# Kernel optimization log

Measured on AMD Instinct MI355X. Metric: run time of the kernel, lower is better.

Reference implementation:

```python
import jax, jax.numpy as jnp
import numpy as np

B, N, C, H = 2, 2048, 1024, 16
D = C // H          # head dim = 64
HID = 4 * C         # MLP hidden = 4096
LN_EPS = 1e-5
ROPE_BASE = 10000.0


def layernorm(x, g, b):
    mu = jnp.mean(x, axis=-1, keepdims=True)
    var = jnp.var(x, axis=-1, keepdims=True)
    return (x - mu) * jax.lax.rsqrt(var + LN_EPS) * g + b


def rotate_half(x):
    # interleaved pairs: (x0, x1) -> (-x1, x0), lucidrains rotary_embedding_torch style
    x = x.reshape(*x.shape[:-1], -1, 2)
    x1, x2 = x[..., 0], x[..., 1]
    return jnp.stack([-x2, x1], axis=-1).reshape(*x.shape[:-2], -1)


def rope_cos_sin(n, d, dtype):
    inv_freq = 1.0 / (ROPE_BASE ** (jnp.arange(0, d, 2, dtype=jnp.float32) / d))
    ang = jnp.arange(n, dtype=jnp.float32)[:, None] * inv_freq          # [N, D/2]
    ang = jnp.repeat(ang, 2, axis=-1)                                    # [N, D] interleaved
    return jnp.cos(ang).astype(dtype), jnp.sin(ang).astype(dtype)


def setup_inputs() -> dict:
    key = jax.random.key(0)
    ks = jax.random.split(key, 16)
    s = 0.02
    return {
        "x": jax.random.normal(ks[0], (B, N, C), jnp.float32),
        "ln1_g": jnp.ones((C,), jnp.float32),
        "ln1_b": jnp.zeros((C,), jnp.float32),
        "qkv_w": jax.random.normal(ks[1], (C, 3 * C), jnp.float32) * s,   # stored [in, out]
        "qkv_b": jnp.zeros((3 * C,), jnp.float32),
        "proj_w": jax.random.normal(ks[2], (C, C), jnp.float32) * s,
        "proj_b": jnp.zeros((C,), jnp.float32),
        "ln2_g": jnp.ones((C,), jnp.float32),
        "ln2_b": jnp.zeros((C,), jnp.float32),
        "fc1_w": jax.random.normal(ks[3], (C, HID), jnp.float32) * s,
        "fc1_b": jnp.zeros((HID,), jnp.float32),
        "ffn_ln_g": jnp.ones((HID,), jnp.float32),
        "ffn_ln_b": jnp.zeros((HID,), jnp.float32),
        "fc2_w": jax.random.normal(ks[4], (HID, C), jnp.float32) * s,
        "fc2_b": jnp.zeros((C,), jnp.float32),
    }


def reference(x, ln1_g, ln1_b, qkv_w, qkv_b, proj_w, proj_b,
              ln2_g, ln2_b, fc1_w, fc1_b, ffn_ln_g, ffn_ln_b, fc2_w, fc2_b):
    b, n, c = x.shape
    h, d = H, c // H
    scale = d ** -0.5

    # --- attention branch (pre-norm) ---
    hx = layernorm(x, ln1_g, ln1_b)
    qkv = hx @ qkv_w + qkv_b                                   # [B,N,3C]
    qkv = qkv.reshape(b, n, 3, h, d).transpose(2, 0, 3, 1, 4)  # [3,B,H,N,D]
    q, k, v = qkv[0], qkv[1], qkv[2]

    cos, sin = rope_cos_sin(n, d, x.dtype)                     # [N,D]
    q = q * cos + rotate_half(q) * sin
    k = k * cos + rotate_half(k) * sin

    attn = jax.nn.softmax(jnp.einsum('bhqd,bhkd->bhqk', q, k) * scale, axis=-1)
    o = jnp.einsum('bhqk,bhkd->bhqd', attn, v)                 # [B,H,N,D]
    o = o.transpose(0, 2, 1, 3).reshape(b, n, c)               # B N (H D)
    x = x + o @ proj_w + proj_b

    # --- MLP branch (pre-norm; GELU then LayerNorm on hidden, per FeedForwardBlock) ---
    m = layernorm(x, ln2_g, ln2_b)
    m = jax.nn.gelu(m @ fc1_w + fc1_b, approximate=False)
    m = layernorm(m, ffn_ln_g, ffn_ln_b)
    m = m @ fc2_w + fc2_b
    return x + m
```

## Files before the change

kernel.cpp:

```cpp
#include <hip/hip_runtime.h>
#include <hip/hip_bf16.h>
#include <cmath>

typedef __bf16 bf16_t;
typedef __bf16 bf16x8 __attribute__((ext_vector_type(8)));
typedef float f32x4 __attribute__((ext_vector_type(4)));
typedef unsigned short u16;
typedef unsigned int u32;

__device__ __forceinline__ void load16(const bf16_t* g, bf16_t* l) {
  __builtin_amdgcn_global_load_lds((const __attribute__((address_space(1))) u32*)g,
                                   (__attribute__((address_space(3))) u32*)l, 16, 0, 0);
}

__device__ __forceinline__ u32 pk2(float a, float b) {
  bf16_t x = (bf16_t)a, y = (bf16_t)b;
  u16 ux = __builtin_bit_cast(u16, x), uy = __builtin_bit_cast(u16, y);
  return (u32)ux | ((u32)uy << 16);
}

union V4U { u32 w[4]; bf16x8 v; };

__global__ __launch_bounds__(256) void transpose_w(const float* __restrict__ Wsrc,
                                                   bf16_t* __restrict__ Wt, int Kd, int Nd) {
  __shared__ float tile[32][33];
  int n0 = blockIdx.x * 32, k0 = blockIdx.y * 32;
  int tx = threadIdx.x & 31, ty = threadIdx.x >> 5;
  for (int i = ty; i < 32; i += 8)
    tile[i][tx] = Wsrc[(size_t)(k0 + i) * Nd + n0 + tx];
  __syncthreads();
  for (int i = ty; i < 32; i += 8)
    Wt[(size_t)(n0 + i) * Kd + k0 + tx] = (bf16_t)tile[tx][i];
}

__global__ void rope_tab(float* __restrict__ c, float* __restrict__ s) {
  int pos = blockIdx.x, t = threadIdx.x;
  float e = (float)(2 * t) / 64.0f;
  float inv = powf(10000.0f, -e);
  float a = (float)pos * inv;
  c[pos * 32 + t] = cosf(a);
  s[pos * 32 + t] = sinf(a);
}

template <typename TI, int W>
__global__ __launch_bounds__(256) void ln_kernel(const TI* __restrict__ in,
                                                 const float* __restrict__ g,
                                                 const float* __restrict__ b,
                                                 bf16_t* __restrict__ out) {
  constexpr int PT = W / 256;
  int row = blockIdx.x;
  const TI* p = in + (size_t)row * W;
  float vals[PT];
  float s = 0.f, q = 0.f;
  for (int i = 0; i < PT; ++i) {
    float v = (float)p[threadIdx.x + i * 256];
    vals[i] = v; s += v; q += v * v;
  }
  for (int off = 32; off; off >>= 1) { s += __shfl_xor(s, off); q += __shfl_xor(q, off); }
  __shared__ float red[8];
  int wave = threadIdx.x >> 6, lane = threadIdx.x & 63;
  if (lane == 0) { red[wave] = s; red[4 + wave] = q; }
  __syncthreads();
  s = red[0] + red[1] + red[2] + red[3];
  q = red[4] + red[5] + red[6] + red[7];
  float mu = s * (1.0f / W);
  float var = q * (1.0f / W) - mu * mu;
  float rstd = rsqrtf(var + 1e-5f);
  bf16_t* op = out + (size_t)row * W;
  for (int i = 0; i < PT; ++i) {
    int cix = threadIdx.x + i * 256;
    op[cix] = (bf16_t)((vals[i] - mu) * rstd * g[cix] + b[cix]);
  }
}

enum { EPI_QKV = 0, EPI_RESID = 1, EPI_GELU = 2 };

template <int EPI>
__global__ __launch_bounds__(256, 2) void gemm_bt(
    const bf16_t* __restrict__ A, const bf16_t* __restrict__ Bt, int M, int Nn, int K,
    const float* __restrict__ bias, const float* __restrict__ resid,
    float* __restrict__ outf, bf16_t* __restrict__ outb,
    bf16_t* __restrict__ qb, bf16_t* __restrict__ kb, bf16_t* __restrict__ vtb,
    const float* __restrict__ ropeC, const float* __restrict__ ropeS) {
  __shared__ bf16_t lsA[128 * 32];
  __shared__ bf16_t lsB[128 * 32];
  const int tid = threadIdx.x;
  const int lane = tid & 63;
  const int wave = tid >> 6;
  const int l16 = lane & 15, quad = lane >> 4;
  const int wm = (wave >> 1) * 64, wn = (wave & 1) * 64;
  const int m0 = blockIdx.y * 128, n0 = blockIdx.x * 128;

  f32x4 acc[4][4];
  for (int i = 0; i < 4; ++i)
    for (int j = 0; j < 4; ++j) acc[i][j] = {0.f, 0.f, 0.f, 0.f};

  for (int kk = 0; kk < K; kk += 32) {
    __syncthreads();
    for (int i = 0; i < 2; ++i) {
      int s = tid + i * 256;
      int row = s >> 2, ch = s & 3;
      load16(A + (size_t)(m0 + row) * K + kk + ch * 8, lsA + s * 8);
      load16(Bt + (size_t)(n0 + row) * K + kk + ch * 8, lsB + s * 8);
    }
    __syncthreads();
    bf16x8 af[4], bfr[4];
    for (int t = 0; t < 4; ++t) {
      af[t] = *(const bf16x8*)(lsA + (wm + t * 16 + l16) * 32 + quad * 8);
      bfr[t] = *(const bf16x8*)(lsB + (wn + t * 16 + l16) * 32 + quad * 8);
    }
    for (int mt = 0; mt < 4; ++mt)
      for (int nt = 0; nt < 4; ++nt)
        acc[mt][nt] = __builtin_amdgcn_mfma_f32_16x16x32_bf16(af[mt], bfr[nt], acc[mt][nt], 0, 0, 0);
  }

  for (int mt = 0; mt < 4; ++mt) {
    for (int nt = 0; nt < 4; ++nt) {
      int gn = n0 + wn + nt * 16 + l16;
      int gm0 = m0 + wm + mt * 16 + quad * 4;
      if constexpr (EPI == EPI_QKV) {
        int which = gn >> 10;
        int hd = gn & 1023, head = hd >> 6, d = hd & 63;
        if (which == 2) {
          u32 lo, hi;
          {
            float v0 = acc[mt][nt][0] + bias[gn];
            float v1 = acc[mt][nt][1] + bias[gn];
            float v2 = acc[mt][nt][2] + bias[gn];
            float v3 = acc[mt][nt][3] + bias[gn];
            lo = pk2(v0, v1);
            hi = pk2(v2, v3);
          }
          int b = gm0 >> 11, pos = gm0 & 2047;
          int bh = b * 16 + head;
          uint2 pk; pk.x = lo; pk.y = hi;
          *(uint2*)(vtb + ((size_t)bh * 64 + d) * 2048 + pos) = pk;
        } else {
          bf16_t* dst = (which == 0) ? qb : kb;
          int t = d >> 1;
          for (int r = 0; r < 4; ++r) {
            float v = acc[mt][nt][r] + bias[gn];
            float pn = __shfl_xor(v, 1);
            int gm = gm0 + r;
            int b = gm >> 11, pos = gm & 2047;
            float cc = ropeC[pos * 32 + t], ss = ropeS[pos * 32 + t];
            float o = (d & 1) ? (v * cc + pn * ss) : (v * cc - pn * ss);
            dst[(((size_t)(b * 16 + head)) * 2048 + pos) * 64 + d] = (bf16_t)o;
          }
        }
      } else if constexpr (EPI == EPI_GELU) {
        for (int r = 0; r < 4; ++r) {
          int gm = gm0 + r;
          float v = acc[mt][nt][r] + bias[gn];
          float g = 0.5f * v * (1.0f + erff(v * 0.70710678118654752f));
          outb[(size_t)gm * Nn + gn] = (bf16_t)g;
        }
      } else {
        for (int r = 0; r < 4; ++r) {
          int gm = gm0 + r;
          size_t idx = (size_t)gm * Nn + gn;
          outf[idx] = acc[mt][nt][r] + bias[gn] + resid[idx];
        }
      }
    }
  }
}

__global__ __launch_bounds__(256, 2) void attn_kernel(
    const bf16_t* __restrict__ q, const bf16_t* __restrict__ k,
    const bf16_t* __restrict__ vt, bf16_t* __restrict__ o) {
  __shared__ bf16_t lsK[128 * 64];
  __shared__ bf16_t lsV[64 * 128];

  const int tid = threadIdx.x, lane = tid & 63, wave = tid >> 6;
  const int l16 = lane & 15, quad = lane >> 4;
  const int bh = blockIdx.y, qt = blockIdx.x;
  const int b = bh >> 4, h = bh & 15;
  const bf16_t* qp = q + (size_t)bh * 2048 * 64;
  const bf16_t* kp = k + (size_t)bh * 2048 * 64;
  const bf16_t* vp = vt + (size_t)bh * 64 * 2048;
  const int qrow0 = qt * 128 + wave * 32;

  bf16x8 qa[2][2];
#pragma unroll
  for (int mt = 0; mt < 2; ++mt)
#pragma unroll
    for (int ks = 0; ks < 2; ++ks) {
      bf16x8 t = *(const bf16x8*)(qp + (size_t)(qrow0 + mt * 16 + l16) * 64 + ks * 32 + quad * 8);
#pragma unroll
      for (int j = 0; j < 8; ++j) t[j] = (bf16_t)((float)t[j] * 0.125f);
      qa[mt][ks] = t;
    }

  f32x4 oacc[2][4];
#pragma unroll
  for (int i = 0; i < 2; ++i)
#pragma unroll
    for (int j = 0; j < 4; ++j) oacc[i][j] = {0.f, 0.f, 0.f, 0.f};
  float mstate[2] = {-1e30f, -1e30f};
  float lstate[2] = {0.f, 0.f};

  for (int kt = 0; kt < 16; ++kt) {
    __syncthreads();
    const bf16_t* kg = kp + (size_t)kt * 128 * 64;
#pragma unroll
    for (int i = 0; i < 4; ++i) {
      int s = tid + i * 256;
      int kr = s >> 3, kc = (s & 7) ^ (kr & 7);
      load16(kg + (size_t)kr * 64 + kc * 8, lsK + s * 8);
      int vr = s >> 4, vc = (s & 15) ^ (vr & 7);
      load16(vp + (size_t)vr * 2048 + kt * 128 + vc * 8, lsV + s * 8);
    }
    __syncthreads();

    f32x4 sacc[8][2];
#pragma unroll
    for (int nt = 0; nt < 8; ++nt)
#pragma unroll
      for (int mt = 0; mt < 2; ++mt) sacc[nt][mt] = {0.f, 0.f, 0.f, 0.f};
#pragma unroll
    for (int ks = 0; ks < 2; ++ks)
#pragma unroll
      for (int nt = 0; nt < 8; ++nt) {
        int rr = nt * 16 + l16;
        int cs = (ks * 4 + quad) ^ (rr & 7);
        bf16x8 kf = *(const bf16x8*)(lsK + rr * 64 + cs * 8);
        sacc[nt][0] = __builtin_amdgcn_mfma_f32_16x16x32_bf16(kf, qa[0][ks], sacc[nt][0], 0, 0, 0);
        sacc[nt][1] = __builtin_amdgcn_mfma_f32_16x16x32_bf16(kf, qa[1][ks], sacc[nt][1], 0, 0, 0);
      }

    u32 u[2][8][2];
#pragma unroll
    for (int mt = 0; mt < 2; ++mt) {
      float mx = sacc[0][mt][0];
#pragma unroll
      for (int nt = 0; nt < 8; ++nt)
#pragma unroll
        for (int r = 0; r < 4; ++r) mx = fmaxf(mx, sacc[nt][mt][r]);
      mx = fmaxf(mx, __shfl_xor(mx, 16));
      mx = fmaxf(mx, __shfl_xor(mx, 32));
      float mnew = fmaxf(mstate[mt], mx);
      float alpha = __expf(mstate[mt] - mnew);
      mstate[mt] = mnew;
      float rs = 0.f;
#pragma unroll
      for (int nt = 0; nt < 8; ++nt) {
        float p0 = __expf(sacc[nt][mt][0] - mnew);
        float p1 = __expf(sacc[nt][mt][1] - mnew);
        float p2 = __expf(sacc[nt][mt][2] - mnew);
        float p3 = __expf(sacc[nt][mt][3] - mnew);
        rs += (p0 + p1) + (p2 + p3);
        u[mt][nt][0] = pk2(p0, p1);
        u[mt][nt][1] = pk2(p2, p3);
      }
      rs += __shfl_xor(rs, 16);
      rs += __shfl_xor(rs, 32);
      lstate[mt] = lstate[mt] * alpha + rs;
#pragma unroll
      for (int r = 0; r < 4; ++r) {
        float a = __shfl(alpha, quad * 4 + r);
#pragma unroll
        for (int dt = 0; dt < 4; ++dt) oacc[mt][dt][r] *= a;
      }
    }

#pragma unroll
    for (int ks = 0; ks < 4; ++ks) {
      bf16x8 pf[2];
#pragma unroll
      for (int mt = 0; mt < 2; ++mt) {
        V4U a;
#pragma unroll
        for (int w = 0; w < 4; ++w) {
          int src = ((quad & 1) * 2 + (w >> 1)) * 16 + l16;
          u32 lo = (u32)__shfl((int)u[mt][2 * ks + 0][w & 1], src);
          u32 hi = (u32)__shfl((int)u[mt][2 * ks + 1][w & 1], src);
          a.w[w] = (quad & 2) ? hi : lo;
        }
        pf[mt] = a.v;
      }
#pragma unroll
      for (int dt = 0; dt < 4; ++dt) {
        int rd = dt * 16 + l16;
        int cs = (ks * 4 + quad) ^ (rd & 7);
        bf16x8 vf = *(const bf16x8*)(lsV + rd * 128 + cs * 8);
        oacc[0][dt] = __builtin_amdgcn_mfma_f32_16x16x32_bf16(pf[0], vf, oacc[0][dt], 0, 0, 0);
        oacc[1][dt] = __builtin_amdgcn_mfma_f32_16x16x32_bf16(pf[1], vf, oacc[1][dt], 0, 0, 0);
      }
    }
  }

#pragma unroll
  for (int mt = 0; mt < 2; ++mt) {
    float inv = 1.0f / lstate[mt];
#pragma unroll
    for (int r = 0; r < 4; ++r) {
      float li = __shfl(inv, quad * 4 + r);
      int row = qrow0 + mt * 16 + quad * 4 + r;
#pragma unroll
      for (int dt = 0; dt < 4; ++dt) {
        int d = dt * 16 + l16;
        o[((size_t)(b * 2048 + row)) * 1024 + h * 64 + d] = (bf16_t)(oacc[mt][dt][r] * li);
      }
    }
  }
}

extern "C" void kernel_launch(void* const* d_in, const int* in_sizes, int n_in,
                              void* d_out, int out_size, void* d_ws, size_t ws_size,
                              hipStream_t stream) {
  const float* x = (const float*)d_in[0];
  const float* ln1_g = (const float*)d_in[1];
  const float* ln1_b = (const float*)d_in[2];
  const float* qkv_w = (const float*)d_in[3];
  const float* qkv_b = (const float*)d_in[4];
  const float* proj_w = (const float*)d_in[5];
  const float* proj_b = (const float*)d_in[6];
  const float* ln2_g = (const float*)d_in[7];
  const float* ln2_b = (const float*)d_in[8];
  const float* fc1_w = (const float*)d_in[9];
  const float* fc1_b = (const float*)d_in[10];
  const float* ffg = (const float*)d_in[11];
  const float* ffb = (const float*)d_in[12];
  const float* fc2_w = (const float*)d_in[13];
  const float* fc2_b = (const float*)d_in[14];
  float* out = (float*)d_out;

  char* ws = (char*)d_ws;
  size_t off = 0;
  auto alloc = [&](size_t n) { char* p = ws + off; off += (n + 255) & ~(size_t)255; return p; };

  bf16_t* qkvT  = (bf16_t*)alloc(3072ull * 1024 * 2);
  bf16_t* projT = (bf16_t*)alloc(1024ull * 1024 * 2);
  bf16_t* fc1T  = (bf16_t*)alloc(4096ull * 1024 * 2);
  bf16_t* fc2T  = (bf16_t*)alloc(1024ull * 4096 * 2);
  float*  ropeC = (float*)alloc(2048ull * 32 * 4);
  float*  ropeS = (float*)alloc(2048ull * 32 * 4);
  bf16_t* hx    = (bf16_t*)alloc(4096ull * 1024 * 2);
  bf16_t* qbuf  = (bf16_t*)alloc(32ull * 2048 * 64 * 2);
  bf16_t* kbuf  = (bf16_t*)alloc(32ull * 2048 * 64 * 2);
  bf16_t* vtbuf = (bf16_t*)alloc(32ull * 64 * 2048 * 2);
  bf16_t* obuf  = (bf16_t*)alloc(4096ull * 1024 * 2);
  float*  x2    = (float*)alloc(4096ull * 1024 * 4);
  bf16_t* h1    = (bf16_t*)alloc(4096ull * 4096 * 2);
  bf16_t* hln   = (bf16_t*)qbuf;

  transpose_w<<<dim3(96, 32), 256, 0, stream>>>(qkv_w, qkvT, 1024, 3072);
  transpose_w<<<dim3(32, 32), 256, 0, stream>>>(proj_w, projT, 1024, 1024);
  transpose_w<<<dim3(128, 32), 256, 0, stream>>>(fc1_w, fc1T, 1024, 4096);
  transpose_w<<<dim3(32, 128), 256, 0, stream>>>(fc2_w, fc2T, 4096, 1024);
  rope_tab<<<2048, 32, 0, stream>>>(ropeC, ropeS);

  ln_kernel<float, 1024><<<4096, 256, 0, stream>>>(x, ln1_g, ln1_b, hx);
  gemm_bt<EPI_QKV><<<dim3(24, 32), 256, 0, stream>>>(hx, qkvT, 4096, 3072, 1024, qkv_b,
      nullptr, nullptr, nullptr, qbuf, kbuf, vtbuf, ropeC, ropeS);
  attn_kernel<<<dim3(16, 32), 256, 0, stream>>>(qbuf, kbuf, vtbuf, obuf);
  gemm_bt<EPI_RESID><<<dim3(8, 32), 256, 0, stream>>>(obuf, projT, 4096, 1024, 1024, proj_b,
      x, x2, nullptr, nullptr, nullptr, nullptr, nullptr, nullptr);
  ln_kernel<float, 1024><<<4096, 256, 0, stream>>>(x2, ln2_g, ln2_b, hx);
  gemm_bt<EPI_GELU><<<dim3(32, 32), 256, 0, stream>>>(hx, fc1T, 4096, 4096, 1024, fc1_b,
      nullptr, nullptr, h1, nullptr, nullptr, nullptr, nullptr, nullptr);
  ln_kernel<bf16_t, 4096><<<4096, 256, 0, stream>>>(h1, ffg, ffb, hln);
  gemm_bt<EPI_RESID><<<dim3(8, 32), 256, 0, stream>>>(hln, fc2T, 4096, 1024, 4096, fc2_b,
      x2, out, nullptr, nullptr, nullptr, nullptr, nullptr, nullptr);
}
```

Measured before the change: 432.2 us.

## Rewrite attention with 32x32 MFMA, double-buffered K/V, exp2 softmax

```diff
diff --git a/kernel.cpp b/kernel.cpp
--- a/kernel.cpp
+++ b/kernel.cpp
@@ -5,6 +5,7 @@
 typedef __bf16 bf16_t;
 typedef __bf16 bf16x8 __attribute__((ext_vector_type(8)));
 typedef float f32x4 __attribute__((ext_vector_type(4)));
+typedef float f32x16 __attribute__((ext_vector_type(16)));
 typedef unsigned short u16;
 typedef unsigned int u32;
 
@@ -169,141 +170,130 @@
 __global__ __launch_bounds__(256, 2) void attn_kernel(
     const bf16_t* __restrict__ q, const bf16_t* __restrict__ k,
     const bf16_t* __restrict__ vt, bf16_t* __restrict__ o) {
-  __shared__ bf16_t lsK[128 * 64];
-  __shared__ bf16_t lsV[64 * 128];
+  __shared__ bf16_t lsK[2][128 * 64];
+  __shared__ bf16_t lsV[2][64 * 128];
 
   const int tid = threadIdx.x, lane = tid & 63, wave = tid >> 6;
-  const int l16 = lane & 15, quad = lane >> 4;
+  const int c31 = lane & 31, hi = lane >> 5, h7 = c31 & 7;
   const int bh = blockIdx.y, qt = blockIdx.x;
   const int b = bh >> 4, h = bh & 15;
   const bf16_t* qp = q + (size_t)bh * 2048 * 64;
   const bf16_t* kp = k + (size_t)bh * 2048 * 64;
   const bf16_t* vp = vt + (size_t)bh * 64 * 2048;
   const int qrow0 = qt * 128 + wave * 32;
-
-  bf16x8 qa[2][2];
-#pragma unroll
-  for (int mt = 0; mt < 2; ++mt)
-#pragma unroll
-    for (int ks = 0; ks < 2; ++ks) {
-      bf16x8 t = *(const bf16x8*)(qp + (size_t)(qrow0 + mt * 16 + l16) * 64 + ks * 32 + quad * 8);
-#pragma unroll
-      for (int j = 0; j < 8; ++j) t[j] = (bf16_t)((float)t[j] * 0.125f);
-      qa[mt][ks] = t;
-    }
-
-  f32x4 oacc[2][4];
-#pragma unroll
-  for (int i = 0; i < 2; ++i)
-#pragma unroll
-    for (int j = 0; j < 4; ++j) oacc[i][j] = {0.f, 0.f, 0.f, 0.f};
-  float mstate[2] = {-1e30f, -1e30f};
-  float lstate[2] = {0.f, 0.f};
-
-  for (int kt = 0; kt < 16; ++kt) {
-    __syncthreads();
+  const int qrow = qrow0 + c31;
+
+  const float QS = 0.18033688011112042f;
+  bf16x8 qb[4];
+#pragma unroll
+  for (int ks = 0; ks < 4; ++ks) {
+    bf16x8 t = *(const bf16x8*)(qp + (size_t)qrow * 64 + ks * 16 + hi * 8);
+#pragma unroll
+    for (int j = 0; j < 8; ++j) t[j] = (bf16_t)((float)t[j] * QS);
+    qb[ks] = t;
+  }
+
+  f32x16 oacc[2];
+  oacc[0] = 0.f; oacc[1] = 0.f;
+  float mstate = -3.0e38f, lstate = 0.f;
+
+  auto stage = [&](int kt, int buf) {
     const bf16_t* kg = kp + (size_t)kt * 128 * 64;
+    bf16_t* lk = &lsK[buf][0];
+    bf16_t* lv = &lsV[buf][0];
 #pragma unroll
     for (int i = 0; i < 4; ++i) {
       int s = tid + i * 256;
       int kr = s >> 3, kc = (s & 7) ^ (kr & 7);
-      load16(kg + (size_t)kr * 64 + kc * 8, lsK + s * 8);
+      load16(kg + (size_t)kr * 64 + kc * 8, lk + s * 8);
       int vr = s >> 4, vc = (s & 15) ^ (vr & 7);
-      load16(vp + (size_t)vr * 2048 + kt * 128 + vc * 8, lsV + s * 8);
-    }
+      load16(vp + (size_t)vr * 2048 + kt * 128 + vc * 8, lv + s * 8);
+    }
+  };
+
+  stage(0, 0);
+  for (int kt = 0; kt < 16; ++kt) {
     __syncthreads();
-
-    f32x4 sacc[8][2];
-#pragma unroll
-    for (int nt = 0; nt < 8; ++nt)
-#pragma unroll
-      for (int mt = 0; mt < 2; ++mt) sacc[nt][mt] = {0.f, 0.f, 0.f, 0.f};
-#pragma unroll
-    for (int ks = 0; ks < 2; ++ks)
-#pragma unroll
-      for (int nt = 0; nt < 8; ++nt) {
-        int rr = nt * 16 + l16;
-        int cs = (ks * 4 + quad) ^ (rr & 7);
-        bf16x8 kf = *(const bf16x8*)(lsK + rr * 64 + cs * 8);
-        sacc[nt][0] = __builtin_amdgcn_mfma_f32_16x16x32_bf16(kf, qa[0][ks], sacc[nt][0], 0, 0, 0);
-        sacc[nt][1] = __builtin_amdgcn_mfma_f32_16x16x32_bf16(kf, qa[1][ks], sacc[nt][1], 0, 0, 0);
+    if (kt < 15) stage(kt + 1, (kt + 1) & 1);
+    const bf16_t* lk = &lsK[kt & 1][0];
+    const bf16_t* lv = &lsV[kt & 1][0];
+
+    f32x16 sacc[4];
+    sacc[0] = 0.f; sacc[1] = 0.f; sacc[2] = 0.f; sacc[3] = 0.f;
+#pragma unroll
+    for (int ks = 0; ks < 4; ++ks) {
+      int cs = ((ks * 2 + hi) ^ h7) * 8;
+#pragma unroll
+      for (int nt = 0; nt < 4; ++nt) {
+        bf16x8 kf = *(const bf16x8*)(lk + (nt * 32 + c31) * 64 + cs);
+        sacc[nt] = __builtin_amdgcn_mfma_f32_32x32x16_bf16(kf, qb[ks], sacc[nt], 0, 0, 0);
       }
-
-    u32 u[2][8][2];
-#pragma unroll
-    for (int mt = 0; mt < 2; ++mt) {
-      float mx = sacc[0][mt][0];
-#pragma unroll
-      for (int nt = 0; nt < 8; ++nt)
-#pragma unroll
-        for (int r = 0; r < 4; ++r) mx = fmaxf(mx, sacc[nt][mt][r]);
-      mx = fmaxf(mx, __shfl_xor(mx, 16));
-      mx = fmaxf(mx, __shfl_xor(mx, 32));
-      float mnew = fmaxf(mstate[mt], mx);
-      float alpha = __expf(mstate[mt] - mnew);
-      mstate[mt] = mnew;
-      float rs = 0.f;
-#pragma unroll
-      for (int nt = 0; nt < 8; ++nt) {
-        float p0 = __expf(sacc[nt][mt][0] - mnew);
-        float p1 = __expf(sacc[nt][mt][1] - mnew);
-        float p2 = __expf(sacc[nt][mt][2] - mnew);
-        float p3 = __expf(sacc[nt][mt][3] - mnew);
+    }
+
+    float mx = sacc[0][0];
+#pragma unroll
+    for (int nt = 0; nt < 4; ++nt)
+#pragma unroll
+      for (int r = 0; r < 16; ++r) mx = fmaxf(mx, sacc[nt][r]);
+    mx = fmaxf(mx, __shfl_xor(mx, 32));
+    float mnew = fmaxf(mstate, mx);
+    float alpha = exp2f(mstate - mnew);
+    mstate = mnew;
+    float rs = 0.f;
+    u32 u[4][4][2];
+#pragma unroll
+    for (int nt = 0; nt < 4; ++nt)
+#pragma unroll
+      for (int t = 0; t < 4; ++t) {
+        float p0 = exp2f(sacc[nt][4 * t + 0] - mnew);
+        float p1 = exp2f(sacc[nt][4 * t + 1] - mnew);
+        float p2 = exp2f(sacc[nt][4 * t + 2] - mnew);
+        float p3 = exp2f(sacc[nt][4 * t + 3] - mnew);
         rs += (p0 + p1) + (p2 + p3);
-        u[mt][nt][0] = pk2(p0, p1);
-        u[mt][nt][1] = pk2(p2, p3);
+        u[nt][t][0] = pk2(p0, p1);
+        u[nt][t][1] = pk2(p2, p3);
       }
-      rs += __shfl_xor(rs, 16);
-      rs += __shfl_xor(rs, 32);
-      lstate[mt] = lstate[mt] * alpha + rs;
-#pragma unroll
-      for (int r = 0; r < 4; ++r) {
-        float a = __shfl(alpha, quad * 4 + r);
-#pragma unroll
-        for (int dt = 0; dt < 4; ++dt) oacc[mt][dt][r] *= a;
+    rs += __shfl_xor(rs, 32);
+    lstate = lstate * alpha + rs;
+#pragma unroll
+    for (int dt = 0; dt < 2; ++dt)
+#pragma unroll
+      for (int r = 0; r < 16; ++r) oacc[dt][r] *= alpha;
+
+#pragma unroll
+    for (int ks = 0; ks < 8; ++ks) {
+      int n = ks >> 1, t0 = (ks & 1) * 2;
+      u32 a0 = u[n][t0][0], a1 = u[n][t0][1];
+      u32 b0 = u[n][t0 + 1][0], b1 = u[n][t0 + 1][1];
+      u32 ax0 = (u32)__shfl_xor((int)a0, 32), ax1 = (u32)__shfl_xor((int)a1, 32);
+      u32 bx0 = (u32)__shfl_xor((int)b0, 32), bx1 = (u32)__shfl_xor((int)b1, 32);
+      V4U f;
+      f.w[0] = hi ? bx0 : a0;
+      f.w[1] = hi ? bx1 : a1;
+      f.w[2] = hi ? b0 : ax0;
+      f.w[3] = hi ? b1 : ax1;
+      bf16x8 pf = f.v;
+      int cs = ((ks * 2 + hi) ^ h7) * 8;
+#pragma unroll
+      for (int dt = 0; dt < 2; ++dt) {
+        bf16x8 vf = *(const bf16x8*)(lv + (dt * 32 + c31) * 128 + cs);
+        oacc[dt] = __builtin_amdgcn_mfma_f32_32x32x16_bf16(vf, pf, oacc[dt], 0, 0, 0);
       }
     }
-
-#pragma unroll
-    for (int ks = 0; ks < 4; ++ks) {
-      bf16x8 pf[2];
-#pragma unroll
-      for (int mt = 0; mt < 2; ++mt) {
-        V4U a;
-#pragma unroll
-        for (int w = 0; w < 4; ++w) {
-          int src = ((quad & 1) * 2 + (w >> 1)) * 16 + l16;
-          u32 lo = (u32)__shfl((int)u[mt][2 * ks + 0][w & 1], src);
-          u32 hi = (u32)__shfl((int)u[mt][2 * ks + 1][w & 1], src);
-          a.w[w] = (quad & 2) ? hi : lo;
-        }
-        pf[mt] = a.v;
-      }
-#pragma unroll
-      for (int dt = 0; dt < 4; ++dt) {
-        int rd = dt * 16 + l16;
-        int cs = (ks * 4 + quad) ^ (rd & 7);
-        bf16x8 vf = *(const bf16x8*)(lsV + rd * 128 + cs * 8);
-        oacc[0][dt] = __builtin_amdgcn_mfma_f32_16x16x32_bf16(pf[0], vf, oacc[0][dt], 0, 0, 0);
-        oacc[1][dt] = __builtin_amdgcn_mfma_f32_16x16x32_bf16(pf[1], vf, oacc[1][dt], 0, 0, 0);
-      }
-    }
-  }
-
-#pragma unroll
-  for (int mt = 0; mt < 2; ++mt) {
-    float inv = 1.0f / lstate[mt];
-#pragma unroll
-    for (int r = 0; r < 4; ++r) {
-      float li = __shfl(inv, quad * 4 + r);
-      int row = qrow0 + mt * 16 + quad * 4 + r;
-#pragma unroll
-      for (int dt = 0; dt < 4; ++dt) {
-        int d = dt * 16 + l16;
-        o[((size_t)(b * 2048 + row)) * 1024 + h * 64 + d] = (bf16_t)(oacc[mt][dt][r] * li);
-      }
-    }
-  }
+  }
+
+  float inv = 1.0f / lstate;
+  bf16_t* orow = o + ((size_t)(b * 2048 + qrow)) * 1024 + h * 64;
+#pragma unroll
+  for (int dt = 0; dt < 2; ++dt)
+#pragma unroll
+    for (int t = 0; t < 4; ++t) {
+      int d0 = dt * 32 + 8 * t + 4 * hi;
+      uint2 pk;
+      pk.x = pk2(oacc[dt][4 * t + 0] * inv, oacc[dt][4 * t + 1] * inv);
+      pk.y = pk2(oacc[dt][4 * t + 2] * inv, oacc[dt][4 * t + 3] * inv);
+      *(uint2*)(orow + d0) = pk;
+    }
 }
 
 extern "C" void kernel_launch(void* const* d_in, const int* in_sizes, int n_in,
```

Result: slower. 447.8 us (+3.6%).
